# Optimization experiments

Hardware: AMD Instinct MI355X
Metric: run time of the kernel (lower is better)

The kernel has to match this reference:

```python
import math
import jax, jax.numpy as jnp
import numpy as np

B, L, S, H, E, D = 2, 2048, 2048, 16, 64, 64

def setup_inputs() -> dict:
    key = jax.random.key(0)
    k1, k2, k3, k4, k5 = jax.random.split(key, 5)
    return {
        "queries": jax.random.normal(k1, (B, L, H, E), dtype=jnp.float32),
        "keys": jax.random.normal(k2, (B, S, H, E), dtype=jnp.float32),
        "values": jax.random.normal(k3, (B, S, H, D), dtype=jnp.float32),
        "tau": jax.random.uniform(k4, (B, 1), dtype=jnp.float32),
        "delta": jax.random.normal(k5, (B, S), dtype=jnp.float32),
        "attn_mask": jnp.zeros((1,), dtype=jnp.bool_),
    }

def reference(queries, keys, values, tau, delta, attn_mask):
    # queries: [B,L,H,E], keys: [B,S,H,E], values: [B,S,H,D]
    # tau: [B,1] -> [B,1,1,1]; delta: [B,S] -> [B,1,1,S]
    # mask_flag=False, so attn_mask is unused. Dropout is identity at eval.
    E_ = queries.shape[-1]
    scale = 1.0 / math.sqrt(E_)
    scores = jnp.einsum('blhe,bshe->bhls', queries, keys)  # [B,H,L,S]
    scores = scores * tau[:, None, None, :]                # de-stationary scale
    scores = scores + delta[:, None, None, :]              # de-stationary shift
    A = jax.nn.softmax(scale * scores, axis=-1)            # [B,H,L,S]
    V = jnp.einsum('bhls,bshd->blhd', A, values)           # [B,L,H,D]
    return V
```

## Files before the change

### kernel.cpp

```cpp
#include <hip/hip_runtime.h>


#define Bb 2
#define Ll 2048
#define Ss 2048
#define Hh 16
#define Ee 64
#define Dd 64
#define KV 64

typedef _Float16 f16x8 __attribute__((ext_vector_type(8)));
typedef _Float16 f16x4 __attribute__((ext_vector_type(4)));
typedef __fp16 fp16x2 __attribute__((ext_vector_type(2)));
typedef float f32x4 __attribute__((ext_vector_type(4)));

union Pk2 { fp16x2 h; unsigned u; };
union PackU { unsigned u[4]; f16x8 v; };

#define GLDS(gp, lp) __builtin_amdgcn_global_load_lds( \
    (const __attribute__((address_space(1))) void*)(gp), \
    (__attribute__((address_space(3))) void*)(lp), 16, 0, 0)

__global__ __launch_bounds__(256)
void prepass_k(const float* __restrict__ K, _Float16* __restrict__ K16,
               const float* __restrict__ delta, float* __restrict__ delta2)
{
    const unsigned v = blockIdx.x * 256 + threadIdx.x;
    const unsigned e4 = v & 15;
    const unsigned h  = (v >> 4) & 15;
    const unsigned s  = (v >> 8) & (Ss - 1);
    const unsigned b  = v >> 19;
    const f32x4 src = ((const f32x4*)K)[v];
    f16x4 t;
    t[0] = (_Float16)src[0]; t[1] = (_Float16)src[1];
    t[2] = (_Float16)src[2]; t[3] = (_Float16)src[3];
    ((f16x4*)K16)[(((size_t)(b * Hh + h) * Ss + s) * 16) + e4] = t;
    if (v < (Bb * Ss) / 4) {
        f32x4 dd = ((const f32x4*)delta)[v];
        ((f32x4*)delta2)[v] = (f32x4){0.125f * dd[0], 0.125f * dd[1],
                                      0.125f * dd[2], 0.125f * dd[3]};
    }
}

__global__ __launch_bounds__(256)
void prepass_v(const float* __restrict__ V, _Float16* __restrict__ VT16)
{
    __shared__ _Float16 TL[64][66];
    const int tid  = threadIdx.x;
    const int wave = tid >> 6;
    const int lane = tid & 63;
    const int bh = blockIdx.y;
    const int b  = bh >> 4;
    const int h  = bh & 15;
    const int s0 = blockIdx.x * 64;

    #pragma unroll
    for (int rr = 0; rr < 16; ++rr) {
        const int row = wave * 16 + rr;
        TL[row][lane] = (_Float16)V[((size_t)(b * Ss + s0 + row) * Hh + h) * Dd + lane];
    }
    __syncthreads();
    const int d  = tid >> 2;
    const int sq = (tid & 3) * 16;
    union { _Float16 h[16]; f16x8 v[2]; } tmp;
    #pragma unroll
    for (int i = 0; i < 16; ++i) tmp.h[i] = TL[sq + i][d];
    f16x8* dp = (f16x8*)(VT16 + ((size_t)(b * Hh + h) * Dd + d) * Ss + s0 + sq);
    dp[0] = tmp.v[0];
    dp[1] = tmp.v[1];
}

__global__ __launch_bounds__(512)
void dsattn_fwd_v7(const float* __restrict__ Q, const _Float16* __restrict__ K16,
                   const _Float16* __restrict__ VT16, const float* __restrict__ tau,
                   const float* __restrict__ delta2, float* __restrict__ out)
{
    extern __shared__ __align__(16) unsigned char smem[];

    const int tid  = threadIdx.x;
    const int wave = tid >> 6;
    const int half = wave >> 2;
    const int wq   = wave & 3;
    const int lane = tid & 63;
    const int lq   = lane & 15;
    const int g    = lane >> 4;
    const int tid_h = tid & 255;

    const int bid = blockIdx.x;
    const int xcd = bid & 7;
    const int kk  = bid >> 3;
    const int bh  = xcd * 4 + (kk & 3);
    const int b   = bh >> 4;
    const int h   = bh & 15;
    const int q0  = (kk >> 2) * 128;
    const int qw  = q0 + wq * 32;

    const float alpha = 0.125f * tau[b];

    f16x8 aq[2][2];
    #pragma unroll
    for (int qg = 0; qg < 2; ++qg) {
        const float* qp = Q + (((size_t)b * Ll + qw + qg * 16 + lq) * Hh + h) * Ee;
        #pragma unroll
        for (int es = 0; es < 2; ++es) {
            const float* p = qp + es * 32 + g * 8;
            f16x8 t;
            #pragma unroll
            for (int j = 0; j < 8; ++j) t[j] = (_Float16)p[j];
            aq[qg][es] = t;
        }
    }

    f32x4 osum[2][4];
    #pragma unroll
    for (int qg = 0; qg < 2; ++qg)
        #pragma unroll
        for (int i = 0; i < 4; ++i) osum[qg][i] = (f32x4){0.f, 0.f, 0.f, 0.f};
    float m_run[2] = {-1e30f, -1e30f};
    float l_run[2] = {0.0f, 0.0f};

    const unsigned char* kb  = (const unsigned char*)(K16 + (size_t)(b * Hh + h) * Ss * Ee);
    const unsigned char* vtb = (const unsigned char*)(VT16 + (size_t)(b * Hh + h) * Dd * Ss);
    const float* d2b = delta2 + (size_t)b * Ss;

    const int row0  = tid_h >> 3;
    const int slotS = (tid_h & 7) ^ (row0 & 7);
    unsigned char* stBase = smem + half * 32768;
    const int sBase = half * (Ss / 2);

    {
        unsigned char* kw = stBase + wq * 1024;
        unsigned char* vw = stBase + 8192 + wq * 1024;
        GLDS(kb + (size_t)(sBase + row0) * 128 + slotS * 16,        kw);
        GLDS(kb + (size_t)(sBase + row0 + 32) * 128 + slotS * 16,   kw + 4096);
        GLDS(vtb + (size_t)row0 * (Ss * 2) + sBase * 2 + slotS * 16,        vw);
        GLDS(vtb + (size_t)(row0 + 32) * (Ss * 2) + sBase * 2 + slotS * 16, vw + 4096);
    }
    f32x4 dcur[4], dnxt[4];
    #pragma unroll
    for (int t = 0; t < 4; ++t)
        dcur[t] = *(const f32x4*)(d2b + sBase + t * 16 + 4 * g);
    __syncthreads();

    const int srcA = lq + 32 * (g & 1);
    const int srcB = srcA + 16;
    const bool gh = (g >> 1);

    int cur = 0;
    for (int it = 0; it < Ss / 2 / KV; ++it) {
        const int sb = sBase + it * KV;
        const int nb = (it + 1 < Ss / 2 / KV);
        if (nb) {
            unsigned char* kw = stBase + (cur ^ 1) * 16384 + wq * 1024;
            unsigned char* vw = kw + 8192;
            const int sn = sb + KV;
            GLDS(kb + (size_t)(sn + row0) * 128 + slotS * 16,        kw);
            GLDS(kb + (size_t)(sn + row0 + 32) * 128 + slotS * 16,   kw + 4096);
            GLDS(vtb + (size_t)row0 * (Ss * 2) + sn * 2 + slotS * 16,        vw);
            GLDS(vtb + (size_t)(row0 + 32) * (Ss * 2) + sn * 2 + slotS * 16, vw + 4096);
        }
        {
            const int sn = nb ? sb + KV : sb;
            #pragma unroll
            for (int t = 0; t < 4; ++t)
                dnxt[t] = *(const f32x4*)(d2b + sn + t * 16 + 4 * g);
        }

        const unsigned char* Ksm = stBase + cur * 16384;
        const unsigned char* Vsm = Ksm + 8192;

        f32x4 c4[2][4];
        #pragma unroll
        for (int qg = 0; qg < 2; ++qg)
            #pragma unroll
            for (int t = 0; t < 4; ++t) c4[qg][t] = (f32x4){0.f, 0.f, 0.f, 0.f};
        __builtin_amdgcn_s_setprio(1);
        #pragma unroll
        for (int t = 0; t < 4; ++t) {
            const int srow = t * 16 + lq;
            #pragma unroll
            for (int es = 0; es < 2; ++es) {
                const int slot = (es * 4 + g) ^ (srow & 7);
                f16x8 ak = *(const f16x8*)(Ksm + srow * 128 + slot * 16);
                c4[0][t] = __builtin_amdgcn_mfma_f32_16x16x32_f16(ak, aq[0][es], c4[0][t], 0, 0, 0);
                c4[1][t] = __builtin_amdgcn_mfma_f32_16x16x32_f16(ak, aq[1][es], c4[1][t], 0, 0, 0);
            }
        }
        __builtin_amdgcn_s_setprio(0);

        PackU bp[2][2];
        #pragma unroll
        for (int qg = 0; qg < 2; ++qg) {
            float p[16];
            float tmax = -1e30f;
            #pragma unroll
            for (int t = 0; t < 4; ++t)
                #pragma unroll
                for (int j = 0; j < 4; ++j) {
                    float z = fmaf(alpha, c4[qg][t][j], dcur[t][j]);
                    p[t * 4 + j] = z;
                    tmax = fmaxf(tmax, z);
                }
            if (!__all(tmax <= m_run[qg] + 8.0f)) {
                float rmax = fmaxf(tmax, __shfl_xor(tmax, 16));
                rmax = fmaxf(rmax, __shfl_xor(rmax, 32));
                const float m_new = fmaxf(m_run[qg], rmax);
                const float corr  = __expf(m_run[qg] - m_new);
                l_run[qg] *= corr;
                #pragma unroll
                for (int dt = 0; dt < 4; ++dt)
                    #pragma unroll
                    for (int j = 0; j < 4; ++j)
                        osum[qg][dt][j] *= corr;
                m_run[qg] = m_new;
            }
            float psum = 0.f;
            #pragma unroll
            for (int i = 0; i < 16; ++i) { p[i] = __expf(p[i] - m_run[qg]); psum += p[i]; }
            l_run[qg] += psum;

            unsigned pk[8];
            #pragma unroll
            for (int t = 0; t < 4; ++t) {
                Pk2 u0, u1;
                u0.h = __builtin_amdgcn_cvt_pkrtz(p[4 * t], p[4 * t + 1]);
                u1.h = __builtin_amdgcn_cvt_pkrtz(p[4 * t + 2], p[4 * t + 3]);
                pk[t * 2] = u0.u;
                pk[t * 2 + 1] = u1.u;
            }
            #pragma unroll
            for (int ks = 0; ks < 2; ++ks) {
                unsigned a0 = __shfl(pk[ks * 4 + 0], srcA), a1 = __shfl(pk[ks * 4 + 1], srcA);
                unsigned a2 = __shfl(pk[ks * 4 + 2], srcA), a3 = __shfl(pk[ks * 4 + 3], srcA);
                unsigned b0 = __shfl(pk[ks * 4 + 0], srcB), b1 = __shfl(pk[ks * 4 + 1], srcB);
                unsigned b2 = __shfl(pk[ks * 4 + 2], srcB), b3 = __shfl(pk[ks * 4 + 3], srcB);
                bp[qg][ks].u[0] = gh ? a2 : a0;
                bp[qg][ks].u[1] = gh ? a3 : a1;
                bp[qg][ks].u[2] = gh ? b2 : b0;
                bp[qg][ks].u[3] = gh ? b3 : b1;
            }
        }

        __builtin_amdgcn_s_setprio(1);
        #pragma unroll
        for (int ks = 0; ks < 2; ++ks)
            #pragma unroll
            for (int dt = 0; dt < 4; ++dt) {
                const int vrow = dt * 16 + lq;
                const int slot = (ks * 4 + g) ^ (vrow & 7);
                f16x8 av = *(const f16x8*)(Vsm + vrow * 128 + slot * 16);
                osum[0][dt] = __builtin_amdgcn_mfma_f32_16x16x32_f16(av, bp[0][ks].v, osum[0][dt], 0, 0, 0);
                osum[1][dt] = __builtin_amdgcn_mfma_f32_16x16x32_f16(av, bp[1][ks].v, osum[1][dt], 0, 0, 0);
            }
        __builtin_amdgcn_s_setprio(0);

        __syncthreads();
        cur ^= 1;
        #pragma unroll
        for (int t = 0; t < 4; ++t) dcur[t] = dnxt[t];
    }

    #pragma unroll
    for (int qg = 0; qg < 2; ++qg) {
        float l = l_run[qg];
        l += __shfl_xor(l, 16);
        l += __shfl_xor(l, 32);
        l_run[qg] = l;
    }

    float (*Part)[2][16][68] = (float (*)[2][16][68])smem;
    if (half == 1) {
        #pragma unroll
        for (int qg = 0; qg < 2; ++qg) {
            #pragma unroll
            for (int dt = 0; dt < 4; ++dt)
                *(f32x4*)&Part[wq][qg][lq][dt * 16 + 4 * g] = osum[qg][dt];
            if (g == 0) {
                Part[wq][qg][lq][64] = m_run[qg];
                Part[wq][qg][lq][65] = l_run[qg];
            }
        }
    }
    __syncthreads();
    if (half == 0) {
        #pragma unroll
        for (int qg = 0; qg < 2; ++qg) {
            const float m1 = Part[wq][qg][lq][64];
            const float l1 = Part[wq][qg][lq][65];
            const float m  = fmaxf(m_run[qg], m1);
            const float s0 = __expf(m_run[qg] - m);
            const float s1 = __expf(m1 - m);
            const float inv = 1.0f / (l_run[qg] * s0 + l1 * s1);
            #pragma unroll
            for (int dt = 0; dt < 4; ++dt) {
                f32x4 p1 = *(const f32x4*)&Part[wq][qg][lq][dt * 16 + 4 * g];
                #pragma unroll
                for (int j = 0; j < 4; ++j)
                    osum[qg][dt][j] = (osum[qg][dt][j] * s0 + p1[j] * s1) * inv;
            }
        }
    }
    __syncthreads();
    float (*Osm)[68] = (float (*)[68])smem;
    if (half == 0) {
        #pragma unroll
        for (int qg = 0; qg < 2; ++qg)
            #pragma unroll
            for (int dt = 0; dt < 4; ++dt)
                *(f32x4*)&Osm[wq * 32 + qg * 16 + lq][dt * 16 + 4 * g] = osum[qg][dt];
    }
    __syncthreads();
    {
        float* ob = out + (((size_t)b * Ll + q0) * Hh + h) * Dd;
        #pragma unroll
        for (int i = 0; i < 16; ++i) {
            const int r = wave * 16 + i;
            ob[(size_t)r * (Hh * Dd) + lane] = Osm[r][lane];
        }
    }
}

__global__ __launch_bounds__(256)
void dsattn_fwd(const float* __restrict__ Q, const float* __restrict__ K,
                const float* __restrict__ V, const float* __restrict__ tau,
                const float* __restrict__ delta, float* __restrict__ out)
{
    __shared__ __align__(16) unsigned char Ksm[32 * 128];
    __shared__ __align__(16) unsigned char VTsm[64 * 80];
    __shared__ float dsm[32];
    __shared__ float Osm[4][16][68];

    const int tid  = threadIdx.x;
    const int wave = tid >> 6;
    const int lane = tid & 63;
    const int lq   = lane & 15;
    const int g    = lane >> 4;

    const int bh = blockIdx.y;
    const int b  = bh >> 4;
    const int h  = bh & 15;
    const int q0 = blockIdx.x * 64;

    const float alpha = 0.125f * tau[b];

    f16x8 aq[2];
    {
        const float* qp = Q + (((long)b * Ll + q0 + wave * 16 + lq) * Hh + h) * Ee;
        #pragma unroll
        for (int es = 0; es < 2; ++es) {
            const float* p = qp + es * 32 + g * 8;
            f16x8 t;
            #pragma unroll
            for (int j = 0; j < 8; ++j) t[j] = (_Float16)p[j];
            aq[es] = t;
        }
    }

    f32x4 osum[4];
    #pragma unroll
    for (int i = 0; i < 4; ++i) osum[i] = (f32x4){0.f, 0.f, 0.f, 0.f};
    float m_run = -1e30f, l_run = 0.0f;

    const float* kb = K + ((long)b * Ss * Hh + h) * Ee;
    const float* vb = V + ((long)b * Ss * Hh + h) * Dd;
    const float* db = delta + (long)b * Ss;

    const int kr    = tid >> 3;
    const int kc    = (tid & 7) * 8;
    const int kslot = (((tid & 7) ^ (kr & 7)) * 16);
    const int vd    = tid & 63;
    const int vsh   = tid >> 6;

    for (int sb = 0; sb < Ss; sb += 32) {
        __syncthreads();
        {
            const float* src = kb + (long)(sb + kr) * (Hh * Ee) + kc;
            f16x8 t;
            #pragma unroll
            for (int j = 0; j < 8; ++j) t[j] = (_Float16)src[j];
            *(f16x8*)(Ksm + kr * 128 + kslot) = t;
        }
        {
            const float* src = vb + (long)(sb + vsh * 8) * (Hh * Dd) + vd;
            f16x8 t;
            #pragma unroll
            for (int j = 0; j < 8; ++j) t[j] = (_Float16)src[j * (Hh * Dd)];
            *(f16x8*)(VTsm + vd * 80 + vsh * 16) = t;
        }
        if (tid < 32) dsm[tid] = 0.125f * db[sb + tid];
        __syncthreads();

        float p[8];
        float tmax = -1e30f;
        #pragma unroll
        for (int t = 0; t < 2; ++t) {
            f32x4 c = (f32x4){0.f, 0.f, 0.f, 0.f};
            #pragma unroll
            for (int es = 0; es < 2; ++es) {
                const int srow = t * 16 + lq;
                const int slot = ((es * 4 + g) ^ (srow & 7)) * 16;
                f16x8 ak = *(const f16x8*)(Ksm + srow * 128 + slot);
                c = __builtin_amdgcn_mfma_f32_16x16x32_f16(ak, aq[es], c, 0, 0, 0);
            }
            #pragma unroll
            for (int j = 0; j < 4; ++j) {
                float z = alpha * c[j] + dsm[t * 16 + 4 * g + j];
                p[t * 4 + j] = z;
                tmax = fmaxf(tmax, z);
            }
        }
        tmax = fmaxf(tmax, __shfl_xor(tmax, 16));
        tmax = fmaxf(tmax, __shfl_xor(tmax, 32));
        const float m_new = fmaxf(m_run, tmax);
        const float corr  = __expf(m_run - m_new);
        float psum = 0.f;
        #pragma unroll
        for (int i = 0; i < 8; ++i) { p[i] = __expf(p[i] - m_new); psum += p[i]; }
        psum += __shfl_xor(psum, 16);
        psum += __shfl_xor(psum, 32);
        l_run = l_run * corr + psum;
        m_run = m_new;
        #pragma unroll
        for (int dt = 0; dt < 4; ++dt)
            #pragma unroll
            for (int j = 0; j < 4; ++j)
                osum[dt][j] *= corr;

        Pk2 u00, u01, u10, u11;
        u00.h = __builtin_amdgcn_cvt_pkrtz(p[0], p[1]);
        u01.h = __builtin_amdgcn_cvt_pkrtz(p[2], p[3]);
        u10.h = __builtin_amdgcn_cvt_pkrtz(p[4], p[5]);
        u11.h = __builtin_amdgcn_cvt_pkrtz(p[6], p[7]);
        const int srcA = lq + 32 * (g & 1);
        const int srcB = srcA + 16;
        unsigned a00 = __shfl(u00.u, srcA), a01 = __shfl(u01.u, srcA);
        unsigned a10 = __shfl(u10.u, srcA), a11 = __shfl(u11.u, srcA);
        unsigned b00 = __shfl(u00.u, srcB), b01 = __shfl(u01.u, srcB);
        unsigned b10 = __shfl(u10.u, srcB), b11 = __shfl(u11.u, srcB);
        const bool hi = (g >= 2);
        PackU bp;
        bp.u[0] = hi ? a10 : a00;
        bp.u[1] = hi ? a11 : a01;
        bp.u[2] = hi ? b10 : b00;
        bp.u[3] = hi ? b11 : b01;

        #pragma unroll
        for (int dt = 0; dt < 4; ++dt) {
            f16x8 av = *(const f16x8*)(VTsm + (dt * 16 + lq) * 80 + g * 16);
            osum[dt] = __builtin_amdgcn_mfma_f32_16x16x32_f16(av, bp.v, osum[dt], 0, 0, 0);
        }
    }

    const float inv = 1.0f / l_run;
    #pragma unroll
    for (int dt = 0; dt < 4; ++dt)
        #pragma unroll
        for (int j = 0; j < 4; ++j)
            Osm[wave][lq][dt * 16 + 4 * g + j] = osum[dt][j] * inv;
    __syncthreads();
    {
        float* ob = out + (((long)b * Ll + q0 + wave * 16) * Hh + h) * Dd;
        #pragma unroll
        for (int r = 0; r < 16; ++r)
            ob[(long)r * (Hh * Dd) + lane] = Osm[wave][r][lane];
    }
}

extern "C" void kernel_launch(void* const* d_in, const int* in_sizes, int n_in,
                              void* d_out, int out_size, void* d_ws, size_t ws_size,
                              hipStream_t stream) {
    const float* Q     = (const float*)d_in[0];
    const float* K     = (const float*)d_in[1];
    const float* V     = (const float*)d_in[2];
    const float* tau   = (const float*)d_in[3];
    const float* delta = (const float*)d_in[4];
    float* out = (float*)d_out;

    const size_t elems = (size_t)Bb * Hh * Ss * Ee;
    const size_t need  = elems * 2 * 2 + (size_t)Bb * Ss * 4;

    if (ws_size >= need) {
        _Float16* K16    = (_Float16*)d_ws;
        _Float16* VT16   = K16 + elems;
        float*    delta2 = (float*)(VT16 + elems);
        hipLaunchKernelGGL(prepass_k, dim3(elems / 4 / 256), dim3(256), 0, stream,
                           K, K16, delta, delta2);
        hipLaunchKernelGGL(prepass_v, dim3(Ss / 64, Bb * Hh), dim3(256), 0, stream, V, VT16);
        hipLaunchKernelGGL(dsattn_fwd_v7, dim3(512), dim3(512), 65536, stream,
                           Q, K16, VT16, tau, delta2, out);
    } else {
        hipLaunchKernelGGL(dsattn_fwd, dim3(Ll / 64, Bb * Hh), dim3(256), 0, stream,
                           Q, K, V, tau, delta, out);
    }
}
```

Before: 89.83 us.

## Software-pipeline QK^T one tile ahead of softmax and switch to exp2

Restructures the attention main loop so the QK^T MFMAs for tile t+1 are issued before the softmax and PV work of tile t. K and V now use separate double-buffered LDS regions with staggered prefetch distances, and the loop is unrolled by two with ping-pong score registers. The softmax is also moved to base-2 by folding log2(e) into the scale and delta, which lets it call the hardware exp2 directly. This aims to hide MFMA latency behind the softmax VALU work, at the cost of extra registers and more complex buffer indexing.

```diff
diff --git a/kernel.cpp b/kernel.cpp
--- a/kernel.cpp
+++ b/kernel.cpp
@@ -8,6 +8,7 @@
 #define Ee 64
 #define Dd 64
 #define KV 64
+#define NT 16
 
 typedef _Float16 f16x8 __attribute__((ext_vector_type(8)));
 typedef _Float16 f16x4 __attribute__((ext_vector_type(4)));
@@ -20,6 +21,14 @@
 #define GLDS(gp, lp) __builtin_amdgcn_global_load_lds( \
     (const __attribute__((address_space(1))) void*)(gp), \
     (__attribute__((address_space(3))) void*)(lp), 16, 0, 0)
+
+#if __has_builtin(__builtin_amdgcn_exp2f)
+#define EXP2(x) __builtin_amdgcn_exp2f(x)
+#else
+#define EXP2(x) exp2f(x)
+#endif
+
+#define LOG2E 1.4426950408889634f
 
 __global__ __launch_bounds__(256)
 void prepass_k(const float* __restrict__ K, _Float16* __restrict__ K16,
@@ -36,9 +45,9 @@
     t[2] = (_Float16)src[2]; t[3] = (_Float16)src[3];
     ((f16x4*)K16)[(((size_t)(b * Hh + h) * Ss + s) * 16) + e4] = t;
     if (v < (Bb * Ss) / 4) {
+        const float sc = 0.125f * LOG2E;
         f32x4 dd = ((const f32x4*)delta)[v];
-        ((f32x4*)delta2)[v] = (f32x4){0.125f * dd[0], 0.125f * dd[1],
-                                      0.125f * dd[2], 0.125f * dd[3]};
+        ((f32x4*)delta2)[v] = (f32x4){sc * dd[0], sc * dd[1], sc * dd[2], sc * dd[3]};
     }
 }
 
@@ -70,8 +79,112 @@
     dp[1] = tmp.v[1];
 }
 
+
+#define PBODY(T, CP, CN, DP, DN)                                                     \
+{                                                                                    \
+    const int sb_ = sBase + (T) * KV;                                                \
+    if ((T) + 2 < NT) {                                                              \
+        unsigned char* kw = stBase + ((T) & 1) * 8192 + wq * 1024;                   \
+        GLDS(kb + (size_t)(sb_ + 2 * KV + row0) * 128 + slotS * 16, kw);             \
+        GLDS(kb + (size_t)(sb_ + 2 * KV + row0 + 32) * 128 + slotS * 16, kw + 4096); \
+    }                                                                                \
+    if ((T) + 1 < NT) {                                                              \
+        unsigned char* vw = stBase + 16384 + (((T) + 1) & 1) * 8192 + wq * 1024;     \
+        GLDS(vtb + (size_t)row0 * (Ss * 2) + (sb_ + KV) * 2 + slotS * 16, vw);       \
+        GLDS(vtb + (size_t)(row0 + 32) * (Ss * 2) + (sb_ + KV) * 2 + slotS * 16, vw + 4096); \
+        _Pragma("unroll")                                                            \
+        for (int q4 = 0; q4 < 4; ++q4)                                               \
+            DN[q4] = *(const f32x4*)(d2b + sb_ + KV + q4 * 16 + 4 * g);              \
+        const unsigned char* Ksm = stBase + (((T) + 1) & 1) * 8192;                  \
+        _Pragma("unroll")                                                            \
+        for (int qg = 0; qg < 2; ++qg)                                               \
+            _Pragma("unroll")                                                        \
+            for (int t4 = 0; t4 < 4; ++t4)                                           \
+                CN[qg][t4] = (f32x4){0.f, 0.f, 0.f, 0.f};                            \
+        __builtin_amdgcn_s_setprio(1);                                               \
+        _Pragma("unroll")                                                            \
+        for (int t4 = 0; t4 < 4; ++t4) {                                             \
+            const int srow = t4 * 16 + lq;                                           \
+            _Pragma("unroll")                                                        \
+            for (int es = 0; es < 2; ++es) {                                         \
+                const int slot = (es * 4 + g) ^ (srow & 7);                          \
+                f16x8 ak = *(const f16x8*)(Ksm + srow * 128 + slot * 16);            \
+                CN[0][t4] = __builtin_amdgcn_mfma_f32_16x16x32_f16(ak, aq[0][es], CN[0][t4], 0, 0, 0); \
+                CN[1][t4] = __builtin_amdgcn_mfma_f32_16x16x32_f16(ak, aq[1][es], CN[1][t4], 0, 0, 0); \
+            }                                                                        \
+        }                                                                            \
+        __builtin_amdgcn_s_setprio(0);                                               \
+    }                                                                                \
+    PackU bp[2][2];                                                                  \
+    _Pragma("unroll")                                                                \
+    for (int qg = 0; qg < 2; ++qg) {                                                 \
+        float p[16];                                                                 \
+        float tmax = -1e30f;                                                         \
+        _Pragma("unroll")                                                            \
+        for (int t4 = 0; t4 < 4; ++t4)                                               \
+            _Pragma("unroll")                                                        \
+            for (int j = 0; j < 4; ++j) {                                            \
+                float z = fmaf(alpha2, CP[qg][t4][j], DP[t4][j]);                    \
+                p[t4 * 4 + j] = z;                                                   \
+                tmax = fmaxf(tmax, z);                                               \
+            }                                                                        \
+        if (!__all(tmax <= m_run[qg] + 11.5416f)) {                                  \
+            float rmax = fmaxf(tmax, __shfl_xor(tmax, 16));                          \
+            rmax = fmaxf(rmax, __shfl_xor(rmax, 32));                                \
+            const float m_new = fmaxf(m_run[qg], rmax);                              \
+            const float corr = EXP2(m_run[qg] - m_new);                              \
+            l_run[qg] *= corr;                                                       \
+            _Pragma("unroll")                                                        \
+            for (int dt = 0; dt < 4; ++dt)                                           \
+                _Pragma("unroll")                                                    \
+                for (int j = 0; j < 4; ++j) osum[qg][dt][j] *= corr;                 \
+            m_run[qg] = m_new;                                                       \
+        }                                                                            \
+        float psum = 0.f;                                                            \
+        _Pragma("unroll")                                                            \
+        for (int i = 0; i < 16; ++i) { p[i] = EXP2(p[i] - m_run[qg]); psum += p[i]; } \
+        l_run[qg] += psum;                                                           \
+        unsigned pk[8];                                                              \
+        _Pragma("unroll")                                                            \
+        for (int t4 = 0; t4 < 4; ++t4) {                                             \
+            Pk2 u0, u1;                                                              \
+            u0.h = __builtin_amdgcn_cvt_pkrtz(p[4 * t4], p[4 * t4 + 1]);             \
+            u1.h = __builtin_amdgcn_cvt_pkrtz(p[4 * t4 + 2], p[4 * t4 + 3]);         \
+            pk[t4 * 2] = u0.u;                                                       \
+            pk[t4 * 2 + 1] = u1.u;                                                   \
+        }                                                                            \
+        _Pragma("unroll")                                                            \
+        for (int ks = 0; ks < 2; ++ks) {                                             \
+            unsigned a0 = __shfl(pk[ks * 4 + 0], srcA), a1 = __shfl(pk[ks * 4 + 1], srcA); \
+            unsigned a2 = __shfl(pk[ks * 4 + 2], srcA), a3 = __shfl(pk[ks * 4 + 3], srcA); \
+            unsigned b0 = __shfl(pk[ks * 4 + 0], srcB), b1 = __shfl(pk[ks * 4 + 1], srcB); \
+            unsigned b2 = __shfl(pk[ks * 4 + 2], srcB), b3 = __shfl(pk[ks * 4 + 3], srcB); \
+            bp[qg][ks].u[0] = gh ? a2 : a0;                                          \
+            bp[qg][ks].u[1] = gh ? a3 : a1;                                          \
+            bp[qg][ks].u[2] = gh ? b2 : b0;                                          \
+            bp[qg][ks].u[3] = gh ? b3 : b1;                                          \
+        }                                                                            \
+    }                                                                                \
+    {                                                                                \
+        const unsigned char* Vsm = stBase + 16384 + ((T) & 1) * 8192;                \
+        __builtin_amdgcn_s_setprio(1);                                               \
+        _Pragma("unroll")                                                            \
+        for (int ks = 0; ks < 2; ++ks)                                               \
+            _Pragma("unroll")                                                        \
+            for (int dt = 0; dt < 4; ++dt) {                                         \
+                const int vrow = dt * 16 + lq;                                       \
+                const int slot = (ks * 4 + g) ^ (vrow & 7);                          \
+                f16x8 av = *(const f16x8*)(Vsm + vrow * 128 + slot * 16);            \
+                osum[0][dt] = __builtin_amdgcn_mfma_f32_16x16x32_f16(av, bp[0][ks].v, osum[0][dt], 0, 0, 0); \
+                osum[1][dt] = __builtin_amdgcn_mfma_f32_16x16x32_f16(av, bp[1][ks].v, osum[1][dt], 0, 0, 0); \
+            }                                                                        \
+        __builtin_amdgcn_s_setprio(0);                                               \
+    }                                                                                \
+    __syncthreads();                                                                 \
+}
+
 __global__ __launch_bounds__(512)
-void dsattn_fwd_v7(const float* __restrict__ Q, const _Float16* __restrict__ K16,
+void dsattn_fwd_v8(const float* __restrict__ Q, const _Float16* __restrict__ K16,
                    const _Float16* __restrict__ VT16, const float* __restrict__ tau,
                    const float* __restrict__ delta2, float* __restrict__ out)
 {
@@ -95,7 +208,7 @@
     const int q0  = (kk >> 2) * 128;
     const int qw  = q0 + wq * 32;
 
-    const float alpha = 0.125f * tau[b];
+    const float alpha2 = 0.125f * LOG2E * tau[b];
 
     f16x8 aq[2][2];
     #pragma unroll
@@ -128,136 +241,51 @@
     unsigned char* stBase = smem + half * 32768;
     const int sBase = half * (Ss / 2);
 
-    {
-        unsigned char* kw = stBase + wq * 1024;
-        unsigned char* vw = stBase + 8192 + wq * 1024;
-        GLDS(kb + (size_t)(sBase + row0) * 128 + slotS * 16,        kw);
-        GLDS(kb + (size_t)(sBase + row0 + 32) * 128 + slotS * 16,   kw + 4096);
-        GLDS(vtb + (size_t)row0 * (Ss * 2) + sBase * 2 + slotS * 16,        vw);
-        GLDS(vtb + (size_t)(row0 + 32) * (Ss * 2) + sBase * 2 + slotS * 16, vw + 4096);
-    }
-    f32x4 dcur[4], dnxt[4];
-    #pragma unroll
-    for (int t = 0; t < 4; ++t)
-        dcur[t] = *(const f32x4*)(d2b + sBase + t * 16 + 4 * g);
-    __syncthreads();
-
     const int srcA = lq + 32 * (g & 1);
     const int srcB = srcA + 16;
     const bool gh = (g >> 1);
 
-    int cur = 0;
-    for (int it = 0; it < Ss / 2 / KV; ++it) {
-        const int sb = sBase + it * KV;
-        const int nb = (it + 1 < Ss / 2 / KV);
-        if (nb) {
-            unsigned char* kw = stBase + (cur ^ 1) * 16384 + wq * 1024;
-            unsigned char* vw = kw + 8192;
-            const int sn = sb + KV;
-            GLDS(kb + (size_t)(sn + row0) * 128 + slotS * 16,        kw);
-            GLDS(kb + (size_t)(sn + row0 + 32) * 128 + slotS * 16,   kw + 4096);
-            GLDS(vtb + (size_t)row0 * (Ss * 2) + sn * 2 + slotS * 16,        vw);
-            GLDS(vtb + (size_t)(row0 + 32) * (Ss * 2) + sn * 2 + slotS * 16, vw + 4096);
-        }
-        {
-            const int sn = nb ? sb + KV : sb;
-            #pragma unroll
-            for (int t = 0; t < 4; ++t)
-                dnxt[t] = *(const f32x4*)(d2b + sn + t * 16 + 4 * g);
-        }
-
-        const unsigned char* Ksm = stBase + cur * 16384;
-        const unsigned char* Vsm = Ksm + 8192;
-
-        f32x4 c4[2][4];
-        #pragma unroll
-        for (int qg = 0; qg < 2; ++qg)
-            #pragma unroll
-            for (int t = 0; t < 4; ++t) c4[qg][t] = (f32x4){0.f, 0.f, 0.f, 0.f};
-        __builtin_amdgcn_s_setprio(1);
-        #pragma unroll
-        for (int t = 0; t < 4; ++t) {
-            const int srow = t * 16 + lq;
+    {
+        unsigned char* kw0 = stBase + wq * 1024;
+        GLDS(kb + (size_t)(sBase + row0) * 128 + slotS * 16, kw0);
+        GLDS(kb + (size_t)(sBase + row0 + 32) * 128 + slotS * 16, kw0 + 4096);
+        unsigned char* vw0 = stBase + 16384 + wq * 1024;
+        GLDS(vtb + (size_t)row0 * (Ss * 2) + sBase * 2 + slotS * 16, vw0);
+        GLDS(vtb + (size_t)(row0 + 32) * (Ss * 2) + sBase * 2 + slotS * 16, vw0 + 4096);
+        unsigned char* kw1 = stBase + 8192 + wq * 1024;
+        GLDS(kb + (size_t)(sBase + KV + row0) * 128 + slotS * 16, kw1);
+        GLDS(kb + (size_t)(sBase + KV + row0 + 32) * 128 + slotS * 16, kw1 + 4096);
+    }
+    f32x4 dA[4], dB[4];
+    #pragma unroll
+    for (int q4 = 0; q4 < 4; ++q4)
+        dA[q4] = *(const f32x4*)(d2b + sBase + q4 * 16 + 4 * g);
+    __syncthreads();
+
+    f32x4 cA[2][4], cB[2][4];
+    #pragma unroll
+    for (int qg = 0; qg < 2; ++qg)
+        #pragma unroll
+        for (int t4 = 0; t4 < 4; ++t4) cA[qg][t4] = (f32x4){0.f, 0.f, 0.f, 0.f};
+    {
+        const unsigned char* Ksm = stBase;
+        #pragma unroll
+        for (int t4 = 0; t4 < 4; ++t4) {
+            const int srow = t4 * 16 + lq;
             #pragma unroll
             for (int es = 0; es < 2; ++es) {
                 const int slot = (es * 4 + g) ^ (srow & 7);
                 f16x8 ak = *(const f16x8*)(Ksm + srow * 128 + slot * 16);
-                c4[0][t] = __builtin_amdgcn_mfma_f32_16x16x32_f16(ak, aq[0][es], c4[0][t], 0, 0, 0);
-                c4[1][t] = __builtin_amdgcn_mfma_f32_16x16x32_f16(ak, aq[1][es], c4[1][t], 0, 0, 0);
+                cA[0][t4] = __builtin_amdgcn_mfma_f32_16x16x32_f16(ak, aq[0][es], cA[0][t4], 0, 0, 0);
+                cA[1][t4] = __builtin_amdgcn_mfma_f32_16x16x32_f16(ak, aq[1][es], cA[1][t4], 0, 0, 0);
             }
         }
-        __builtin_amdgcn_s_setprio(0);
-
-        PackU bp[2][2];
-        #pragma unroll
-        for (int qg = 0; qg < 2; ++qg) {
-            float p[16];
-            float tmax = -1e30f;
-            #pragma unroll
-            for (int t = 0; t < 4; ++t)
-                #pragma unroll
-                for (int j = 0; j < 4; ++j) {
-                    float z = fmaf(alpha, c4[qg][t][j], dcur[t][j]);
-                    p[t * 4 + j] = z;
-                    tmax = fmaxf(tmax, z);
-                }
-            if (!__all(tmax <= m_run[qg] + 8.0f)) {
-                float rmax = fmaxf(tmax, __shfl_xor(tmax, 16));
-                rmax = fmaxf(rmax, __shfl_xor(rmax, 32));
-                const float m_new = fmaxf(m_run[qg], rmax);
-                const float corr  = __expf(m_run[qg] - m_new);
-                l_run[qg] *= corr;
-                #pragma unroll
-                for (int dt = 0; dt < 4; ++dt)
-                    #pragma unroll
-                    for (int j = 0; j < 4; ++j)
-                        osum[qg][dt][j] *= corr;
-                m_run[qg] = m_new;
-            }
-            float psum = 0.f;
-            #pragma unroll
-            for (int i = 0; i < 16; ++i) { p[i] = __expf(p[i] - m_run[qg]); psum += p[i]; }
-            l_run[qg] += psum;
-
-            unsigned pk[8];
-            #pragma unroll
-            for (int t = 0; t < 4; ++t) {
-                Pk2 u0, u1;
-                u0.h = __builtin_amdgcn_cvt_pkrtz(p[4 * t], p[4 * t + 1]);
-                u1.h = __builtin_amdgcn_cvt_pkrtz(p[4 * t + 2], p[4 * t + 3]);
-                pk[t * 2] = u0.u;
-                pk[t * 2 + 1] = u1.u;
-            }
-            #pragma unroll
-            for (int ks = 0; ks < 2; ++ks) {
-                unsigned a0 = __shfl(pk[ks * 4 + 0], srcA), a1 = __shfl(pk[ks * 4 + 1], srcA);
-                unsigned a2 = __shfl(pk[ks * 4 + 2], srcA), a3 = __shfl(pk[ks * 4 + 3], srcA);
-                unsigned b0 = __shfl(pk[ks * 4 + 0], srcB), b1 = __shfl(pk[ks * 4 + 1], srcB);
-                unsigned b2 = __shfl(pk[ks * 4 + 2], srcB), b3 = __shfl(pk[ks * 4 + 3], srcB);
-                bp[qg][ks].u[0] = gh ? a2 : a0;
-                bp[qg][ks].u[1] = gh ? a3 : a1;
-                bp[qg][ks].u[2] = gh ? b2 : b0;
-                bp[qg][ks].u[3] = gh ? b3 : b1;
-            }
-        }
-
-        __builtin_amdgcn_s_setprio(1);
-        #pragma unroll
-        for (int ks = 0; ks < 2; ++ks)
-            #pragma unroll
-            for (int dt = 0; dt < 4; ++dt) {
-                const int vrow = dt * 16 + lq;
-                const int slot = (ks * 4 + g) ^ (vrow & 7);
-                f16x8 av = *(const f16x8*)(Vsm + vrow * 128 + slot * 16);
-                osum[0][dt] = __builtin_amdgcn_mfma_f32_16x16x32_f16(av, bp[0][ks].v, osum[0][dt], 0, 0, 0);
-                osum[1][dt] = __builtin_amdgcn_mfma_f32_16x16x32_f16(av, bp[1][ks].v, osum[1][dt], 0, 0, 0);
-            }
-        __builtin_amdgcn_s_setprio(0);
-
-        __syncthreads();
-        cur ^= 1;
-        #pragma unroll
-        for (int t = 0; t < 4; ++t) dcur[t] = dnxt[t];
+    }
+    __syncthreads();
+
+    for (int t = 0; t < NT; t += 2) {
+        PBODY(t,     cA, cB, dA, dB);
+        PBODY(t + 1, cB, cA, dB, dA);
     }
 
     #pragma unroll
@@ -288,8 +316,8 @@
             const float m1 = Part[wq][qg][lq][64];
             const float l1 = Part[wq][qg][lq][65];
             const float m  = fmaxf(m_run[qg], m1);
-            const float s0 = __expf(m_run[qg] - m);
-            const float s1 = __expf(m1 - m);
+            const float s0 = EXP2(m_run[qg] - m);
+            const float s1 = EXP2(m1 - m);
             const float inv = 1.0f / (l_run[qg] * s0 + l1 * s1);
             #pragma unroll
             for (int dt = 0; dt < 4; ++dt) {
@@ -486,7 +514,7 @@
         hipLaunchKernelGGL(prepass_k, dim3(elems / 4 / 256), dim3(256), 0, stream,
                            K, K16, delta, delta2);
         hipLaunchKernelGGL(prepass_v, dim3(Ss / 64, Bb * Hh), dim3(256), 0, stream, V, VT16);
-        hipLaunchKernelGGL(dsattn_fwd_v7, dim3(512), dim3(512), 65536, stream,
+        hipLaunchKernelGGL(dsattn_fwd_v8, dim3(512), dim3(512), 65536, stream,
                            Q, K16, VT16, tau, delta2, out);
     } else {
         hipLaunchKernelGGL(dsattn_fwd, dim3(Ll / 64, Bb * Hh), dim3(256), 0, stream,
```

New measurement: 86.96 us. -3.2%, faster.
